# Kernel tuning notes

Measured on AMD Instinct MI355X. Metric: run time of the kernel, lower is better.

Reference implementation:

```python
import jax, jax.numpy as jnp
import numpy as np

BLOCK_SIZE = 16
E2M1_LOOKUP = jnp.array([0.0, 0.5, 1.0, 1.5, 2.0, 3.0, 4.0, 6.0], dtype=jnp.float32)


def setup_inputs() -> dict:
    key = jax.random.key(0)
    k1, k2, k3, k4, k5 = jax.random.split(key, 5)
    in_features, out_features = 8192, 8192
    x = jax.random.normal(k1, (64, in_features), dtype=jnp.float32)
    weight_packed = jax.random.randint(k2, (out_features, in_features // 2), 0, 256, dtype=jnp.int32)
    weight_scale = jax.random.uniform(k3, (out_features, in_features // BLOCK_SIZE), dtype=jnp.float32)
    weight_global_scale = jax.random.uniform(k4, (1,), dtype=jnp.float32) + 0.5
    bias = jax.random.normal(k5, (out_features,), dtype=jnp.float32)
    return {"x": x, "weight_packed": weight_packed, "weight_scale": weight_scale,
            "weight_global_scale": weight_global_scale, "bias": bias}


def unpack_nvfp4(weight_packed, weight_scale, weight_global_scale, dtype=jnp.float32):
    out_features, in_packed = weight_packed.shape
    in_features = in_packed * 2
    low = weight_packed & 15
    high = (weight_packed >> 4) & 15
    # per-byte order: low nibble first, then high nibble
    combined = jnp.stack([low, high], axis=-1).reshape(out_features, in_features)
    signs = (combined >> 3) & 1
    mag_idx = combined & 7
    values = E2M1_LOOKUP[mag_idx] * (1.0 - 2.0 * signs.astype(jnp.float32))
    # per-block (16-wide) scale
    values = (values.reshape(out_features, -1, BLOCK_SIZE) * weight_scale[..., None]).reshape(out_features, in_features)
    g = weight_global_scale.reshape(())
    actual_scale = jnp.where(g != 0, 1.0 / g, 1.0)
    return (values * actual_scale).astype(dtype)


def reference(x, weight_packed, weight_scale, weight_global_scale, bias):
    W = unpack_nvfp4(weight_packed, weight_scale, weight_global_scale, dtype=x.dtype)
    return x @ W.T + bias
```

## Files before the change

### kernel.cpp

```cpp
#include <hip/hip_runtime.h>
#include <stdint.h>

typedef _Float16 f16x2 __attribute__((ext_vector_type(2)));
typedef _Float16 f16x8 __attribute__((ext_vector_type(8)));
typedef float f32x4 __attribute__((ext_vector_type(4)));

static __device__ __forceinline__ uint32_t perm(uint32_t hi, uint32_t lo, uint32_t sel) {
    return __builtin_amdgcn_perm(hi, lo, sel);
}
static __device__ __forceinline__ f16x2 bch2(uint32_t u) { union { uint32_t x; f16x2 h; } c; c.x = u; return c.h; }
static __device__ __forceinline__ uint32_t bcu(f16x2 h) { union { uint32_t x; f16x2 h; } c; c.h = h; return c.x; }
static __device__ __forceinline__ uint32_t pkrtz(float a, float b) {
    auto r = __builtin_amdgcn_cvt_pkrtz(a, b);
    union { decltype(r) h; uint32_t u; } c; c.h = r; return c.u;
}

#define NTOT 8192
#define KTOT 8192
#define SPLITS 16
#define KCHUNK 512
#define BN 256

__global__ __launch_bounds__(256, 2) void nvfp4_init_out(const float* __restrict__ bias,
                                                         float* __restrict__ out) {
    int i = blockIdx.x * 256 + threadIdx.x;
    ((f32x4*)out)[i] = ((const f32x4*)bias)[i & 2047];
}

__global__ __launch_bounds__(512, 4) void nvfp4_gemm(const float* __restrict__ x,
                                                     const int* __restrict__ wp,
                                                     const float* __restrict__ ws,
                                                     const float* __restrict__ gs,
                                                     float* __restrict__ out) {
    __shared__ __align__(16) uint8_t xl[64 * 256 * 2];
    __shared__ uint32_t sl[256 * 33];

    const int tid = threadIdx.x;
    const int nb = blockIdx.x & 31;
    const int ksp = blockIdx.x >> 5;
    const int nbase = nb * BN;
    const int kc0 = ksp * KCHUNK;

    {
        float g = gs[0];
        float inv_g = (g != 0.0f) ? (1.0f / g) : 1.0f;
        int row = tid >> 1;
        int cb = (tid & 1) * 16;
        const f32x4* sp = (const f32x4*)(ws + (size_t)(nbase + row) * 512 + (kc0 >> 4) + cb);
        uint32_t* d = sl + row * 33 + cb;
        #pragma unroll
        for (int q = 0; q < 4; ++q) {
            f32x4 v = sp[q];
            float a0 = v.x * inv_g, a1 = v.y * inv_g, a2 = v.z * inv_g, a3 = v.w * inv_g;
            d[q * 4 + 0] = pkrtz(a0, a0);
            d[q * 4 + 1] = pkrtz(a1, a1);
            d[q * 4 + 2] = pkrtz(a2, a2);
            d[q * 4 + 3] = pkrtz(a3, a3);
        }
    }

    const int lane = tid & 63;
    const int wid = tid >> 6;
    const int l15 = lane & 15;
    const int grp = lane >> 4;

    auto stage_x = [&](int h) {
        int a = tid >> 5;
        int cb8 = (tid & 31) * 8;
        const float* xp = x + (size_t)a * KTOT + kc0 + h * 256 + cb8;
        #pragma unroll
        for (int j = 0; j < 4; ++j) {
            int row = a + j * 16;
            f32x4 v0 = *(const f32x4*)(xp + (size_t)j * 16 * KTOT);
            f32x4 v1 = *(const f32x4*)(xp + (size_t)j * 16 * KTOT + 4);
            uint4 d;
            d.x = pkrtz(v0.x, v0.y);
            d.y = pkrtz(v0.z, v0.w);
            d.z = pkrtz(v1.x, v1.y);
            d.w = pkrtz(v1.z, v1.w);
            uint32_t addr = ((uint32_t)(row * 512 + cb8 * 2)) ^ ((row & 7) << 4);
            *(uint4*)(xl + addr) = d;
        }
    };

    f32x4 acc[4][2];
    #pragma unroll
    for (int a = 0; a < 4; ++a)
        #pragma unroll
        for (int b = 0; b < 2; ++b)
            acc[a][b] = f32x4{0.f, 0.f, 0.f, 0.f};

    const uint32_t TH = 0x46444240u, TL = 0x3E3C3800u;

    const int wrow0 = nbase + wid * 32 + l15;
    const int* wp0 = wp + (size_t)wrow0 * 4096 + (kc0 >> 1) + grp * 4;
    const int* wp1 = wp + (size_t)(wrow0 + 16) * 4096 + (kc0 >> 1) + grp * 4;
    const int srow0 = (wid * 32 + l15) * 33;
    const int srow1 = (wid * 32 + 16 + l15) * 33;

    stage_x(0);
    int4 wc0 = *(const int4*)(wp0);
    int4 wc1 = *(const int4*)(wp1);
    __syncthreads();

    #pragma unroll
    for (int t = 0; t < 16; ++t) {
        if (t == 8) {
            __syncthreads();
            stage_x(1);
            __syncthreads();
        }
        int4 wn0, wn1;
        if (t < 15) {
            wn0 = *(const int4*)(wp0 + (t + 1) * 16);
            wn1 = *(const int4*)(wp1 + (t + 1) * 16);
        }
        f16x8 af[4];
        #pragma unroll
        for (int mt = 0; mt < 4; ++mt) {
            int row = mt * 16 + l15;
            uint32_t addr = ((uint32_t)(row * 512 + ((t & 7) * 32 + grp * 8) * 2)) ^ ((row & 7) << 4);
            af[mt] = *(const f16x8*)(xl + addr);
        }
        const int scol = t * 2 + (grp >> 1);
        f16x2 s2a = bch2(sl[srow0 + scol]);
        f16x2 s2b = bch2(sl[srow1 + scol]);

        #pragma unroll
        for (int ss = 0; ss < 2; ++ss) {
            const int4 w4 = ss ? wc1 : wc0;
            const f16x2 s2 = ss ? s2b : s2a;
            uint32_t b = (uint32_t)(w4.x & 0xff) | ((uint32_t)(w4.y & 0xff) << 8) |
                         ((uint32_t)(w4.z & 0xff) << 16) | ((uint32_t)w4.w << 24);
            uint32_t sel_e = b & 0x07070707u;
            uint32_t sel_o = (b >> 4) & 0x07070707u;
            uint32_t he = perm(TH, TL, sel_e) | ((b & 0x08080808u) << 4);
            uint32_t ho = perm(TH, TL, sel_o) | (b & 0x80808080u);
            uint32_t d0 = perm(ho, he, 0x040C000Cu);
            uint32_t d1 = perm(ho, he, 0x050C010Cu);
            uint32_t d2 = perm(ho, he, 0x060C020Cu);
            uint32_t d3 = perm(ho, he, 0x070C030Cu);
            union { uint32_t u[4]; f16x8 h; } fr;
            fr.u[0] = bcu(bch2(d0) * s2);
            fr.u[1] = bcu(bch2(d1) * s2);
            fr.u[2] = bcu(bch2(d2) * s2);
            fr.u[3] = bcu(bch2(d3) * s2);
            #pragma unroll
            for (int mt = 0; mt < 4; ++mt)
                acc[mt][ss] = __builtin_amdgcn_mfma_f32_16x16x32_f16(af[mt], fr.h, acc[mt][ss], 0, 0, 0);
        }
        wc0 = wn0;
        wc1 = wn1;
    }

    #pragma unroll
    for (int mt = 0; mt < 4; ++mt)
        #pragma unroll
        for (int ss = 0; ss < 2; ++ss)
            #pragma unroll
            for (int q = 0; q < 4; ++q) {
                int row = mt * 16 + grp * 4 + q;
                int col = nbase + wid * 32 + ss * 16 + l15;
                unsafeAtomicAdd(out + (size_t)row * NTOT + col, acc[mt][ss][q]);
            }
}

extern "C" void kernel_launch(void* const* d_in, const int* in_sizes, int n_in,
                              void* d_out, int out_size, void* d_ws, size_t ws_size,
                              hipStream_t stream) {
    const float* x = (const float*)d_in[0];
    const int* wp = (const int*)d_in[1];
    const float* ws = (const float*)d_in[2];
    const float* gs = (const float*)d_in[3];
    const float* bias = (const float*)d_in[4];
    float* out = (float*)d_out;

    nvfp4_init_out<<<dim3(512), dim3(256), 0, stream>>>(bias, out);
    nvfp4_gemm<<<dim3(SPLITS * (NTOT / BN)), dim3(512), 0, stream>>>(x, wp, ws, gs, out);
}
```

Measured before the change: 235.7 us.

## Halve split-K, double-buffer x staging, and reduce partials without atomics

Split-K drops from 16 to 8 chunks of 1024, which halves the blocks and the redundant x staging. x tiles are now double-buffered in shared memory with register prefetch, and weight loads run two steps ahead through a 3-deep ring, so fewer barriers stall the loop. When the workspace is large enough, partial sums go to the workspace and a separate reduce kernel adds the bias, replacing the atomic adds. The cost is lower parallelism with 256 blocks, more LDS per block (about 130KB, so one block per CU), and extra memory traffic for the partials.

```diff
diff --git a/kernel.cpp b/kernel.cpp
--- a/kernel.cpp
+++ b/kernel.cpp
@@ -17,9 +17,10 @@
 
 #define NTOT 8192
 #define KTOT 8192
-#define SPLITS 16
-#define KCHUNK 512
+#define SPLITS 8
+#define KCHUNK 1024
 #define BN 256
+#define QK 256
 
 __global__ __launch_bounds__(256, 2) void nvfp4_init_out(const float* __restrict__ bias,
                                                          float* __restrict__ out) {
@@ -27,13 +28,27 @@
     ((f32x4*)out)[i] = ((const f32x4*)bias)[i & 2047];
 }
 
-__global__ __launch_bounds__(512, 4) void nvfp4_gemm(const float* __restrict__ x,
+__global__ __launch_bounds__(256, 2) void nvfp4_reduce(const float* __restrict__ part,
+                                                       const float* __restrict__ bias,
+                                                       float* __restrict__ out) {
+    int i = blockIdx.x * 256 + threadIdx.x;
+    f32x4 s = ((const f32x4*)bias)[i & 2047];
+    #pragma unroll
+    for (int p = 0; p < SPLITS; ++p) {
+        f32x4 v = ((const f32x4*)part)[(size_t)p * 131072 + i];
+        s = s + v;
+    }
+    ((f32x4*)out)[i] = s;
+}
+
+__global__ __launch_bounds__(512, 2) void nvfp4_gemm(const float* __restrict__ x,
                                                      const int* __restrict__ wp,
-                                                     const float* __restrict__ ws,
+                                                     const float* __restrict__ wscale,
                                                      const float* __restrict__ gs,
-                                                     float* __restrict__ out) {
-    __shared__ __align__(16) uint8_t xl[64 * 256 * 2];
-    __shared__ uint32_t sl[256 * 33];
+                                                     float* __restrict__ dst,
+                                                     int atomic_mode) {
+    __shared__ __align__(16) uint8_t xl[2][64 * 256 * 2];
+    __shared__ uint32_t sl[256 * 65];
 
     const int tid = threadIdx.x;
     const int nb = blockIdx.x & 31;
@@ -45,11 +60,11 @@
         float g = gs[0];
         float inv_g = (g != 0.0f) ? (1.0f / g) : 1.0f;
         int row = tid >> 1;
-        int cb = (tid & 1) * 16;
-        const f32x4* sp = (const f32x4*)(ws + (size_t)(nbase + row) * 512 + (kc0 >> 4) + cb);
-        uint32_t* d = sl + row * 33 + cb;
-        #pragma unroll
-        for (int q = 0; q < 4; ++q) {
+        int cb = (tid & 1) * 32;
+        const f32x4* sp = (const f32x4*)(wscale + (size_t)(nbase + row) * 512 + ksp * 64 + cb);
+        uint32_t* d = sl + row * 65 + cb;
+        #pragma unroll
+        for (int q = 0; q < 8; ++q) {
             f32x4 v = sp[q];
             float a0 = v.x * inv_g, a1 = v.y * inv_g, a2 = v.z * inv_g, a3 = v.w * inv_g;
             d[q * 4 + 0] = pkrtz(a0, a0);
@@ -64,22 +79,29 @@
     const int l15 = lane & 15;
     const int grp = lane >> 4;
 
-    auto stage_x = [&](int h) {
-        int a = tid >> 5;
-        int cb8 = (tid & 31) * 8;
-        const float* xp = x + (size_t)a * KTOT + kc0 + h * 256 + cb8;
+    const int sa = tid >> 5;
+    const int scb = (tid & 31) * 8;
+    const float* xbase = x + (size_t)sa * KTOT + kc0 + scb;
+
+    auto xload = [&](int q, f32x4* r) {
+        const float* p = xbase + q * QK;
         #pragma unroll
         for (int j = 0; j < 4; ++j) {
-            int row = a + j * 16;
-            f32x4 v0 = *(const f32x4*)(xp + (size_t)j * 16 * KTOT);
-            f32x4 v1 = *(const f32x4*)(xp + (size_t)j * 16 * KTOT + 4);
+            r[j * 2 + 0] = *(const f32x4*)(p + (size_t)j * 16 * KTOT);
+            r[j * 2 + 1] = *(const f32x4*)(p + (size_t)j * 16 * KTOT + 4);
+        }
+    };
+    auto xwrite = [&](int b, const f32x4* r) {
+        #pragma unroll
+        for (int j = 0; j < 4; ++j) {
+            int row = sa + j * 16;
             uint4 d;
-            d.x = pkrtz(v0.x, v0.y);
-            d.y = pkrtz(v0.z, v0.w);
-            d.z = pkrtz(v1.x, v1.y);
-            d.w = pkrtz(v1.z, v1.w);
-            uint32_t addr = ((uint32_t)(row * 512 + cb8 * 2)) ^ ((row & 7) << 4);
-            *(uint4*)(xl + addr) = d;
+            d.x = pkrtz(r[j * 2].x, r[j * 2].y);
+            d.y = pkrtz(r[j * 2].z, r[j * 2].w);
+            d.z = pkrtz(r[j * 2 + 1].x, r[j * 2 + 1].y);
+            d.w = pkrtz(r[j * 2 + 1].z, r[j * 2 + 1].w);
+            uint32_t addr = ((uint32_t)(row * 512 + scb * 2)) ^ ((row & 7) << 4);
+            *(uint4*)(xl[b] + addr) = d;
         }
     };
 
@@ -93,34 +115,36 @@
     const uint32_t TH = 0x46444240u, TL = 0x3E3C3800u;
 
     const int wrow0 = nbase + wid * 32 + l15;
-    const int* wp0 = wp + (size_t)wrow0 * 4096 + (kc0 >> 1) + grp * 4;
-    const int* wp1 = wp + (size_t)(wrow0 + 16) * 4096 + (kc0 >> 1) + grp * 4;
-    const int srow0 = (wid * 32 + l15) * 33;
-    const int srow1 = (wid * 32 + 16 + l15) * 33;
-
-    stage_x(0);
-    int4 wc0 = *(const int4*)(wp0);
-    int4 wc1 = *(const int4*)(wp1);
+    const int* wq0 = wp + (size_t)wrow0 * 4096 + (kc0 >> 1) + grp * 4;
+    const int* wq1 = wp + (size_t)(wrow0 + 16) * 4096 + (kc0 >> 1) + grp * 4;
+    const int srow0 = (wid * 32 + l15) * 65;
+    const int srow1 = (wid * 32 + 16 + l15) * 65;
+
+    f32x4 sA[8], sB[8];
+    xload(0, sA);
+    int4 w0[3], w1[3];
+    w0[0] = *(const int4*)(wq0);
+    w1[0] = *(const int4*)(wq1);
+    w0[1] = *(const int4*)(wq0 + 16);
+    w1[1] = *(const int4*)(wq1 + 16);
+    xwrite(0, sA);
+    xload(1, sB);
     __syncthreads();
 
     #pragma unroll
-    for (int t = 0; t < 16; ++t) {
-        if (t == 8) {
-            __syncthreads();
-            stage_x(1);
-            __syncthreads();
-        }
-        int4 wn0, wn1;
-        if (t < 15) {
-            wn0 = *(const int4*)(wp0 + (t + 1) * 16);
-            wn1 = *(const int4*)(wp1 + (t + 1) * 16);
+    for (int t = 0; t < 32; ++t) {
+        const int rb = (t >> 3) & 1;
+        const int tq = t & 7;
+        if (t < 30) {
+            w0[(t + 2) % 3] = *(const int4*)(wq0 + (t + 2) * 16);
+            w1[(t + 2) % 3] = *(const int4*)(wq1 + (t + 2) * 16);
         }
         f16x8 af[4];
         #pragma unroll
         for (int mt = 0; mt < 4; ++mt) {
             int row = mt * 16 + l15;
-            uint32_t addr = ((uint32_t)(row * 512 + ((t & 7) * 32 + grp * 8) * 2)) ^ ((row & 7) << 4);
-            af[mt] = *(const f16x8*)(xl + addr);
+            uint32_t addr = ((uint32_t)(row * 512 + (tq * 32 + grp * 8) * 2)) ^ ((row & 7) << 4);
+            af[mt] = *(const f16x8*)(xl[rb] + addr);
         }
         const int scol = t * 2 + (grp >> 1);
         f16x2 s2a = bch2(sl[srow0 + scol]);
@@ -128,7 +152,7 @@
 
         #pragma unroll
         for (int ss = 0; ss < 2; ++ss) {
-            const int4 w4 = ss ? wc1 : wc0;
+            const int4 w4 = ss ? w1[t % 3] : w0[t % 3];
             const f16x2 s2 = ss ? s2b : s2a;
             uint32_t b = (uint32_t)(w4.x & 0xff) | ((uint32_t)(w4.y & 0xff) << 8) |
                          ((uint32_t)(w4.z & 0xff) << 16) | ((uint32_t)w4.w << 24);
@@ -149,20 +173,40 @@
             for (int mt = 0; mt < 4; ++mt)
                 acc[mt][ss] = __builtin_amdgcn_mfma_f32_16x16x32_f16(af[mt], fr.h, acc[mt][ss], 0, 0, 0);
         }
-        wc0 = wn0;
-        wc1 = wn1;
-    }
-
-    #pragma unroll
-    for (int mt = 0; mt < 4; ++mt)
-        #pragma unroll
-        for (int ss = 0; ss < 2; ++ss)
+
+        if ((t & 7) == 7 && t < 31) {
+            const int q = t >> 3;
+            if (q == 0) { xwrite(1, sB); xload(2, sA); }
+            if (q == 1) { xwrite(0, sA); xload(3, sB); }
+            if (q == 2) { xwrite(1, sB); }
+            __syncthreads();
+        }
+    }
+
+    if (atomic_mode) {
+        #pragma unroll
+        for (int mt = 0; mt < 4; ++mt)
             #pragma unroll
-            for (int q = 0; q < 4; ++q) {
-                int row = mt * 16 + grp * 4 + q;
-                int col = nbase + wid * 32 + ss * 16 + l15;
-                unsafeAtomicAdd(out + (size_t)row * NTOT + col, acc[mt][ss][q]);
-            }
+            for (int ss = 0; ss < 2; ++ss)
+                #pragma unroll
+                for (int q = 0; q < 4; ++q) {
+                    int row = mt * 16 + grp * 4 + q;
+                    int col = nbase + wid * 32 + ss * 16 + l15;
+                    unsafeAtomicAdd(dst + (size_t)row * NTOT + col, acc[mt][ss][q]);
+                }
+    } else {
+        float* pd = dst + (size_t)ksp * 64 * NTOT;
+        #pragma unroll
+        for (int mt = 0; mt < 4; ++mt)
+            #pragma unroll
+            for (int ss = 0; ss < 2; ++ss)
+                #pragma unroll
+                for (int q = 0; q < 4; ++q) {
+                    int row = mt * 16 + grp * 4 + q;
+                    int col = nbase + wid * 32 + ss * 16 + l15;
+                    pd[(size_t)row * NTOT + col] = acc[mt][ss][q];
+                }
+    }
 }
 
 extern "C" void kernel_launch(void* const* d_in, const int* in_sizes, int n_in,
@@ -170,11 +214,17 @@
                               hipStream_t stream) {
     const float* x = (const float*)d_in[0];
     const int* wp = (const int*)d_in[1];
-    const float* ws = (const float*)d_in[2];
+    const float* wscale = (const float*)d_in[2];
     const float* gs = (const float*)d_in[3];
     const float* bias = (const float*)d_in[4];
     float* out = (float*)d_out;
 
-    nvfp4_init_out<<<dim3(512), dim3(256), 0, stream>>>(bias, out);
-    nvfp4_gemm<<<dim3(SPLITS * (NTOT / BN)), dim3(512), 0, stream>>>(x, wp, ws, gs, out);
-}
+    const size_t need = (size_t)SPLITS * 64 * NTOT * sizeof(float);
+    if (ws_size >= need) {
+        nvfp4_gemm<<<dim3(SPLITS * (NTOT / BN)), dim3(512), 0, stream>>>(x, wp, wscale, gs, (float*)d_ws, 0);
+        nvfp4_reduce<<<dim3(512), dim3(256), 0, stream>>>((const float*)d_ws, bias, out);
+    } else {
+        nvfp4_init_out<<<dim3(512), dim3(256), 0, stream>>>(bias, out);
+        nvfp4_gemm<<<dim3(SPLITS * (NTOT / BN)), dim3(512), 0, stream>>>(x, wp, wscale, gs, out, 1);
+    }
+}
```

Measured after the change: 221.4 us. -6.1%, faster.
